# Performance work log

Measured on AMD Instinct MI355X. Metric: run time of the kernel, lower is better.

The kernel has to match this reference:

```python
import jax, jax.numpy as jnp
import numpy as np

N_NODES = 100000
N_EDGES = 1600000
F_IN = 65
HIDDEN = 128
N_CLASSES = 32
NEG_SLOPE = 0.2


def _gat_conv(x0, src, dst, W, a_src, a_dst, b):
    """Single-head GAT-style conv: gather over edges, segment softmax, scatter-add."""
    h = x0 @ W                                  # [N, C]
    s = h @ a_src                                # [N]
    d = h @ a_dst                                # [N]
    e = jax.nn.leaky_relu(s[src] + d[dst], NEG_SLOPE)   # [E]
    m = jax.ops.segment_max(e, dst, num_segments=N_NODES)
    m = jnp.where(jnp.isfinite(m), m, 0.0)
    ex = jnp.exp(e - m[dst])                     # [E]
    denom = jax.ops.segment_sum(ex, dst, num_segments=N_NODES)
    alpha = ex / (denom[dst] + 1e-16)            # [E]
    out = jax.ops.segment_sum(h[src] * alpha[:, None], dst, num_segments=N_NODES)
    return out + b                               # [N, C]


def setup_inputs() -> dict:
    key = jax.random.key(0)
    ks = jax.random.split(key, 12)
    sc_in = 1.0 / np.sqrt(F_IN)
    sc_h = 1.0 / np.sqrt(HIDDEN)
    return {
        "x": jax.random.normal(ks[0], (N_NODES, F_IN), dtype=jnp.float32),
        "edge_index": jax.random.randint(ks[1], (2, N_EDGES), 0, N_NODES, dtype=jnp.int64),
        "W_mlp": jax.random.normal(ks[2], (F_IN, HIDDEN), dtype=jnp.float32) * sc_in,
        "b_mlp": jnp.zeros((HIDDEN,), dtype=jnp.float32),
        "W1": jax.random.normal(ks[3], (HIDDEN, N_CLASSES), dtype=jnp.float32) * sc_h,
        "a1_src": jax.random.normal(ks[4], (N_CLASSES,), dtype=jnp.float32) * 0.1,
        "a1_dst": jax.random.normal(ks[5], (N_CLASSES,), dtype=jnp.float32) * 0.1,
        "b1": jnp.zeros((N_CLASSES,), dtype=jnp.float32),
        "W2": jax.random.normal(ks[6], (HIDDEN, N_CLASSES), dtype=jnp.float32) * sc_h,
        "a2_src": jax.random.normal(ks[7], (N_CLASSES,), dtype=jnp.float32) * 0.1,
        "a2_dst": jax.random.normal(ks[8], (N_CLASSES,), dtype=jnp.float32) * 0.1,
        "b2": jnp.zeros((N_CLASSES,), dtype=jnp.float32),
    }


def reference(x, edge_index, W_mlp, b_mlp, W1, a1_src, a1_dst, b1, W2, a2_src, a2_dst, b2):
    src, dst = edge_index[0], edge_index[1]
    x0 = jax.nn.relu(x @ W_mlp + b_mlp)                      # [N, H]
    x1 = jax.nn.relu(_gat_conv(x0, src, dst, W1, a1_src, a1_dst, b1))  # [N, C]
    # dropout is identity in eval mode
    x2 = _gat_conv(x0, src, dst, W2, a2_src, a2_dst, b2)     # [N, C]
    x3 = jnp.max(x0, axis=-1, keepdims=True)                 # [N, 1]
    lngal_out = jnp.concatenate((x1, x2, x3), axis=-1) + x   # [N, 2C+1] == [N, F]
    return jax.nn.log_softmax(lngal_out, axis=1)
```

## Files before the change

### kernel.cpp

```cpp
#include <hip/hip_runtime.h>
#include <hip/hip_bf16.h>

#define NN 100000
#define NE 1600000
#define FIN 65
#define HID 128
#define NC 32
#define OUTC 65
#define NBUCK 391
#define CHUNKS 400
#define CH 4000
#define ESTRIDE 5120
#define NODE_BLOCKS 1563

typedef __attribute__((ext_vector_type(8))) short s8v;
typedef __attribute__((ext_vector_type(4))) float f4v;
typedef __attribute__((ext_vector_type(2))) float f2v;
#define MFMA16(a, b, c) __builtin_amdgcn_mfma_f32_16x16x32_bf16(a, b, c, 0, 0, 0)

__device__ __forceinline__ float lrelu(float v){ return v > 0.f ? v : 0.2f * v; }
__device__ __forceinline__ short f2bs(float f){
  unsigned u = __float_as_uint(f);
  u += 0x7fffu + ((u >> 16) & 1u);
  return (short)(u >> 16);
}
__device__ __forceinline__ float bfu_lo(unsigned u){ return __uint_as_float(u << 16); }
__device__ __forceinline__ float bfu_hi(unsigned u){ return __uint_as_float(u & 0xffff0000u); }
__device__ __forceinline__ unsigned char f2fp8(float f){
  int p = __builtin_amdgcn_cvt_pk_fp8_f32(f, f, 0, false);
  return (unsigned char)(p & 0xff);
}

__global__ __launch_bounds__(256) void k_prep(
    const float* __restrict__ Wmlp, const float* __restrict__ W1,
    const float* __restrict__ W2, short* __restrict__ wbg,
    int* __restrict__ bcursor)
{
  const int i = blockIdx.x * 256 + threadIdx.x;
  if (blockIdx.x == 0)
    for (int t = threadIdx.x; t < NBUCK; t += 256) bcursor[t] = 0;
  {
    const int j = i & 7, l = (i >> 3) & 63, nt = (i >> 9) & 7, t = i >> 12;
    const int k = t * 32 + ((l >> 4) << 3) + j;
    const int col = (nt << 4) + (l & 15);
    wbg[i] = f2bs(Wmlp[k * HID + col]);
  }
  {
    const int j = i & 7, l = (i >> 3) & 63, nt = (i >> 9) & 3, t = i >> 11;
    const int k = t * 32 + ((l >> 4) << 3) + j;
    const int col = (nt << 4) + (l & 15);
    wbg[8192 + i] = f2bs(col < NC ? W1[k * NC + col] : W2[k * NC + col - NC]);
  }
}

__global__ __launch_bounds__(256) void k_main(
    const float* __restrict__ x, const short* __restrict__ wbg,
    const float* __restrict__ Wmlp, const float* __restrict__ bmlp,
    const float* __restrict__ a1s, const float* __restrict__ a1d,
    const float* __restrict__ a2s, const float* __restrict__ a2d,
    const int* __restrict__ ei,
    unsigned char* __restrict__ hb8,
    float* __restrict__ sd2, float* __restrict__ dd2,
    float* __restrict__ out,
    int* __restrict__ bcursor, int* __restrict__ ebuf)
{
  __shared__ alignas(16) char smem[18944];
  const int tid = threadIdx.x;

  if (blockIdx.x >= NODE_BLOCKS) {
    const int cb = blockIdx.x - NODE_BLOCKS;
    int* lh = (int*)smem;
    int* lbase = lh + NBUCK;
    for (int i = tid; i < NBUCK; i += 256) lh[i] = 0;
    __syncthreads();
    const int4* s4 = (const int4*)ei + cb * (CH / 4);
    const int4* d4 = (const int4*)(ei + NE) + cb * (CH / 4);
    for (int i = tid; i < CH / 4; i += 256) {
      int4 v = d4[i];
      atomicAdd(&lh[v.x >> 8], 1);
      atomicAdd(&lh[v.y >> 8], 1);
      atomicAdd(&lh[v.z >> 8], 1);
      atomicAdd(&lh[v.w >> 8], 1);
    }
    __syncthreads();
    for (int i = tid; i < NBUCK; i += 256) {
      int c = lh[i];
      lbase[i] = c ? (i * ESTRIDE + atomicAdd(&bcursor[i], c)) : 0;
      lh[i] = 0;
    }
    __syncthreads();
    for (int i = tid; i < CH / 4; i += 256) {
      int4 sv = s4[i];
      int4 dv = d4[i];
      int b, r;
      b = dv.x >> 8; r = atomicAdd(&lh[b], 1); ebuf[lbase[b] + r] = (sv.x << 8) | (dv.x & 255);
      b = dv.y >> 8; r = atomicAdd(&lh[b], 1); ebuf[lbase[b] + r] = (sv.y << 8) | (dv.y & 255);
      b = dv.z >> 8; r = atomicAdd(&lh[b], 1); ebuf[lbase[b] + r] = (sv.z << 8) | (dv.z & 255);
      b = dv.w >> 8; r = atomicAdd(&lh[b], 1); ebuf[lbase[b] + r] = (sv.w << 8) | (dv.w & 255);
    }
    return;
  }

  short* x0b = (short*)smem;
  float* w64 = (float*)(smem + 17408);
  float* bmv = (float*)(smem + 17920);
  float* avv = (float*)(smem + 18432);

  const int base = blockIdx.x * 64;
  const int w = tid >> 6, lane = tid & 63;
  const int g = lane >> 4, q = lane & 15;
  const int rowA = w * 16 + q;
  const int rowD0 = w * 16 + g * 4;
  const int nodeA = base + rowA;
  const s8v* wv8 = (const s8v*)wbg;

  float xa[16];
  if (nodeA < NN) {
    const float* xr = x + (size_t)nodeA * FIN + g * 8;
    #pragma unroll
    for (int j = 0; j < 8; ++j) xa[j] = xr[j];
    #pragma unroll
    for (int j = 0; j < 8; ++j) xa[8 + j] = xr[32 + j];
  } else {
    #pragma unroll
    for (int j = 0; j < 16; ++j) xa[j] = 0.f;
  }
  float xc[4];
  #pragma unroll
  for (int r = 0; r < 4; ++r) {
    const int n2 = base + rowD0 + r;
    xc[r] = (n2 < NN) ? x[(size_t)n2 * FIN + 64] : 0.f;
  }

  if (tid < 128) { w64[tid] = Wmlp[64 * HID + tid]; bmv[tid] = bmlp[tid]; }
  else if (tid < 160) {
    const int qq = tid - 128;
    avv[qq] = a1s[qq]; avv[32 + qq] = a1d[qq]; avv[64 + qq] = a2s[qq]; avv[96 + qq] = a2d[qq];
  }
  __syncthreads();

  s8v a0, a1;
  #pragma unroll
  for (int j = 0; j < 8; ++j) { a0[j] = f2bs(xa[j]); a1[j] = f2bs(xa[8 + j]); }

  f4v acc[8];
  #pragma unroll
  for (int nt = 0; nt < 8; ++nt) acc[nt] = (f4v){0.f, 0.f, 0.f, 0.f};
  {
    s8v bb[8];
    #pragma unroll
    for (int nt = 0; nt < 8; ++nt) bb[nt] = wv8[nt * 64 + lane];
    #pragma unroll
    for (int nt = 0; nt < 8; ++nt) acc[nt] = MFMA16(a0, bb[nt], acc[nt]);
    #pragma unroll
    for (int nt = 0; nt < 8; ++nt) bb[nt] = wv8[(8 + nt) * 64 + lane];
    #pragma unroll
    for (int nt = 0; nt < 8; ++nt) acc[nt] = MFMA16(a1, bb[nt], acc[nt]);
  }

  float rmax[4] = {0.f, 0.f, 0.f, 0.f};
  #pragma unroll
  for (int nt = 0; nt < 8; ++nt) {
    const int col = nt * 16 + q;
    const float wvv = w64[col], bv = bmv[col];
    #pragma unroll
    for (int r = 0; r < 4; ++r) {
      const float v = fmaxf(fmaf(xc[r], wvv, acc[nt][r]) + bv, 0.f);
      rmax[r] = fmaxf(rmax[r], v);
      x0b[(rowD0 + r) * 136 + col] = f2bs(v);
    }
  }
  #pragma unroll
  for (int off = 1; off < 16; off <<= 1)
    #pragma unroll
    for (int r = 0; r < 4; ++r) rmax[r] = fmaxf(rmax[r], __shfl_xor(rmax[r], off));
  if (q == 0) {
    #pragma unroll
    for (int r = 0; r < 4; ++r) {
      const int node = base + rowD0 + r;
      if (node < NN) out[(size_t)node * OUTC + 64] = rmax[r];
    }
  }

  s8v af[4];
  #pragma unroll
  for (int t2 = 0; t2 < 4; ++t2)
    af[t2] = *(const s8v*)&x0b[rowA * 136 + t2 * 32 + g * 8];
  f4v hacc[4];
  #pragma unroll
  for (int nt = 0; nt < 4; ++nt) hacc[nt] = (f4v){0.f, 0.f, 0.f, 0.f};
  {
    s8v wt[8];
    #pragma unroll
    for (int i2 = 0; i2 < 8; ++i2) wt[i2] = wv8[1024 + i2 * 64 + lane];
    #pragma unroll
    for (int t2 = 0; t2 < 2; ++t2)
      #pragma unroll
      for (int nt = 0; nt < 4; ++nt)
        hacc[nt] = MFMA16(af[t2], wt[t2 * 4 + nt], hacc[nt]);
    #pragma unroll
    for (int i2 = 0; i2 < 8; ++i2) wt[i2] = wv8[1024 + (8 + i2) * 64 + lane];
    #pragma unroll
    for (int t2 = 0; t2 < 2; ++t2)
      #pragma unroll
      for (int nt = 0; nt < 4; ++nt)
        hacc[nt] = MFMA16(af[2 + t2], wt[t2 * 4 + nt], hacc[nt]);
  }

  float s1p[4], d1p[4], s2p[4], d2p[4];
  #pragma unroll
  for (int r = 0; r < 4; ++r) {
    s1p[r] = hacc[0][r] * avv[q]        + hacc[1][r] * avv[16 + q];
    d1p[r] = hacc[0][r] * avv[32 + q]   + hacc[1][r] * avv[48 + q];
    s2p[r] = hacc[2][r] * avv[64 + q]   + hacc[3][r] * avv[80 + q];
    d2p[r] = hacc[2][r] * avv[96 + q]   + hacc[3][r] * avv[112 + q];
  }
  #pragma unroll
  for (int off = 1; off < 16; off <<= 1) {
    #pragma unroll
    for (int r = 0; r < 4; ++r) {
      s1p[r] += __shfl_xor(s1p[r], off);
      d1p[r] += __shfl_xor(d1p[r], off);
      s2p[r] += __shfl_xor(s2p[r], off);
      d2p[r] += __shfl_xor(d2p[r], off);
    }
  }
  #pragma unroll
  for (int r = 0; r < 4; ++r) {
    const int node = base + rowD0 + r;
    if (node < NN) {
      #pragma unroll
      for (int nt = 0; nt < 4; ++nt)
        hb8[(size_t)node * 64 + nt * 16 + q] = f2fp8(hacc[nt][r]);
      if (q == 0) {
        *(float2*)&sd2[(size_t)node * 2] = make_float2(s1p[r], s2p[r]);
        *(float2*)&dd2[(size_t)node * 2] = make_float2(d1p[r], d2p[r]);
      }
    }
  }
}

__global__ __launch_bounds__(256) void k_csr(const int* __restrict__ bcursor,
                                             const int* __restrict__ ebuf,
                                             int* __restrict__ rpp,
                                             int* __restrict__ csrc)
{
  __shared__ int lh[256];
  __shared__ int wsum[4];
  const int b = blockIdx.x;
  const int e0 = b * ESTRIDE;
  const int cntb = bcursor[b];
  const int t = threadIdx.x;

  lh[t] = 0;
  __syncthreads();
  for (int i = t; i < cntb; i += 256)
    atomicAdd(&lh[ebuf[e0 + i] & 255], 1);
  __syncthreads();

  const int lane = t & 63;
  const int wid = t >> 6;
  int v = lh[t];
  const int orig = v;
  for (int off = 1; off < 64; off <<= 1) {
    int tm = __shfl_up(v, off);
    if (lane >= off) v += tm;
  }
  if (lane == 63) wsum[wid] = v;
  __syncthreads();
  int add = 0;
  for (int ww = 0; ww < wid; ++ww) add += wsum[ww];
  const int ex = v + add - orig;

  const int nb0 = b << 8;
  if (nb0 + t < NN) rpp[nb0 + t] = ((e0 + ex) << 8) | orig;
  __syncthreads();
  lh[t] = ex;
  __syncthreads();
  for (int i = t; i < cntb; i += 256) {
    int p = ebuf[e0 + i];
    int r = atomicAdd(&lh[p & 255], 1);
    csrc[e0 + r] = ((unsigned)p) >> 8;
  }
}

__global__ __launch_bounds__(256) void k_conv(
    const int* __restrict__ rpp, const int* __restrict__ csrc,
    const unsigned char* __restrict__ hb8,
    const float* __restrict__ sd2, const float* __restrict__ dd2,
    const float* __restrict__ x,
    const float* __restrict__ b1, const float* __restrict__ b2,
    float* __restrict__ out)
{
  const int wid = threadIdx.x >> 6;
  const int lane = threadIdx.x & 63;
  const int half = lane >> 5;
  const int hl = lane & 31;
  const int eg = hl >> 4;
  const int cg = hl & 15;
  const int conv = cg >> 3;

  const int node = blockIdx.x * 8 + wid * 2 + half;

  const int rv = rpp[node];
  const int base = ((unsigned)rv) >> 8;
  const int cnt = rv & 255;
  const float2 dnv = *(const float2*)&dd2[(size_t)node * 2];

  const int ch = cg * 4;
  const float* xr = x + (size_t)node * OUTC;
  float* row = out + (size_t)node * OUTC;
  const float4 xr4 = *(const float4*)&xr[ch];
  const float x64v = xr[64];
  const float o64 = row[64];
  const float4 bv = conv ? *(const float4*)&b2[ch - 32] : *(const float4*)&b1[ch];

  float a0 = 0.f, a1 = 0.f, a2 = 0.f, a3 = 0.f;
  float den = 0.f;

  for (int chunk = 0; chunk < cnt; chunk += 32) {
    const int rem = min(cnt - chunk, 32);

    int sE = 0;
    float w1v = 0.f, w2v = 0.f;
    if (hl < rem) {
      sE = csrc[base + chunk + hl];
      const float2 sv = *(const float2*)&sd2[(size_t)sE * 2];
      w1v = __expf(lrelu(sv.x + dnv.x));
      w2v = __expf(lrelu(sv.y + dnv.y));
    }
    float d1 = w1v, d2 = w2v;
    #pragma unroll
    for (int off = 1; off < 32; off <<= 1) {
      d1 += __shfl_xor(d1, off);
      d2 += __shfl_xor(d2, off);
    }
    den += conv ? d2 : d1;

    const int wpk = (int)((((unsigned)(unsigned short)f2bs(w2v)) << 16) |
                           (unsigned)(unsigned short)f2bs(w1v));

    for (int i0 = 0; i0 < rem; i0 += 8) {
      unsigned wps[4];
      unsigned pvs[4];
      #pragma unroll
      for (int u = 0; u < 4; ++u) {
        const int i = i0 + u * 2 + eg;
        const int src = half * 32 + i;
        const int s = __shfl(sE, src);
        wps[u] = (unsigned)__shfl(wpk, src);
        pvs[u] = *(const unsigned*)(hb8 + ((size_t)s << 6) + cg * 4);
      }
      #pragma unroll
      for (int u = 0; u < 4; ++u) {
        const float w = conv ? bfu_hi(wps[u]) : bfu_lo(wps[u]);
        const f2v lo = __builtin_amdgcn_cvt_pk_f32_fp8((int)pvs[u], false);
        const f2v hi = __builtin_amdgcn_cvt_pk_f32_fp8((int)pvs[u], true);
        a0 = fmaf(w, lo[0], a0);
        a1 = fmaf(w, lo[1], a1);
        a2 = fmaf(w, hi[0], a2);
        a3 = fmaf(w, hi[1], a3);
      }
    }
  }

  a0 += __shfl_xor(a0, 16);
  a1 += __shfl_xor(a1, 16);
  a2 += __shfl_xor(a2, 16);
  a3 += __shfl_xor(a3, 16);

  const float rden = 1.f / (den + 1e-16f);
  float v0 = a0 * rden + bv.x;
  float v1 = a1 * rden + bv.y;
  float v2 = a2 * rden + bv.z;
  float v3 = a3 * rden + bv.w;
  if (conv == 0) {
    v0 = fmaxf(v0, 0.f);
    v1 = fmaxf(v1, 0.f);
    v2 = fmaxf(v2, 0.f);
    v3 = fmaxf(v3, 0.f);
  }
  v0 += xr4.x; v1 += xr4.y; v2 += xr4.z; v3 += xr4.w;
  const float v64 = o64 + x64v;

  float mx = fmaxf(fmaxf(v0, v1), fmaxf(v2, v3));
  #pragma unroll
  for (int off = 1; off < 16; off <<= 1) mx = fmaxf(mx, __shfl_xor(mx, off));
  mx = fmaxf(mx, v64);
  float sm = __expf(v0 - mx) + __expf(v1 - mx) + __expf(v2 - mx) + __expf(v3 - mx);
  #pragma unroll
  for (int off = 1; off < 16; off <<= 1) sm += __shfl_xor(sm, off);
  sm += __expf(v64 - mx);
  const float ls = __logf(sm);

  if (eg == 0) {
    *(float4*)&row[ch] = make_float4(v0 - mx - ls, v1 - mx - ls, v2 - mx - ls, v3 - mx - ls);
    if (hl == 0) row[64] = v64 - mx - ls;
  }
}

extern "C" void kernel_launch(void* const* d_in, const int* in_sizes, int n_in,
                              void* d_out, int out_size, void* d_ws, size_t ws_size,
                              hipStream_t stream)
{
  const float* x    = (const float*)d_in[0];
  const int*   ei   = (const int*)d_in[1];
  const float* Wmlp = (const float*)d_in[2];
  const float* bmlp = (const float*)d_in[3];
  const float* W1   = (const float*)d_in[4];
  const float* a1s  = (const float*)d_in[5];
  const float* a1d  = (const float*)d_in[6];
  const float* b1   = (const float*)d_in[7];
  const float* W2   = (const float*)d_in[8];
  const float* a2s  = (const float*)d_in[9];
  const float* a2d  = (const float*)d_in[10];
  const float* b2   = (const float*)d_in[11];
  float* out = (float*)d_out;

  unsigned char* hb8 = (unsigned char*)d_ws;
  float* sd2 = (float*)(hb8 + (size_t)NN * 64);
  float* dd2 = sd2 + (size_t)2 * NN;
  int* ebuf   = (int*)(dd2 + (size_t)2 * NN);
  int* csrc   = ebuf + (size_t)NBUCK * ESTRIDE;
  int* rpp    = csrc + (size_t)NBUCK * ESTRIDE;
  int* bcursor= rpp + NBUCK * 256;
  short* wbg  = (short*)(bcursor + NBUCK);

  k_prep<<<32, 256, 0, stream>>>(Wmlp, W1, W2, wbg, bcursor);

  k_main<<<NODE_BLOCKS + CHUNKS, 256, 0, stream>>>(
      x, wbg, Wmlp, bmlp, a1s, a1d, a2s, a2d, ei,
      hb8, sd2, dd2, out, bcursor, ebuf);

  k_csr<<<NBUCK, 256, 0, stream>>>(bcursor, ebuf, rpp, csrc);

  k_conv<<<NN / 8, 256, 0, stream>>>(rpp, csrc, hb8, sd2, dd2, x, b1, b2, out);
}
```

Measured before the change: 90.94 us.

## Single-pass edge bucketing with LDS staging and schedule edge blocks first

```diff
diff --git a/kernel.cpp b/kernel.cpp
--- a/kernel.cpp
+++ b/kernel.cpp
@@ -12,6 +12,7 @@
 #define CH 4000
 #define ESTRIDE 5120
 #define NODE_BLOCKS 1563
+#define CAP 16
 
 typedef __attribute__((ext_vector_type(8))) short s8v;
 typedef __attribute__((ext_vector_type(4))) float f4v;
@@ -64,39 +65,49 @@
     float* __restrict__ out,
     int* __restrict__ bcursor, int* __restrict__ ebuf)
 {
-  __shared__ alignas(16) char smem[18944];
+  __shared__ alignas(16) char smem[26624];
   const int tid = threadIdx.x;
 
-  if (blockIdx.x >= NODE_BLOCKS) {
-    const int cb = blockIdx.x - NODE_BLOCKS;
+  if (blockIdx.x < CHUNKS) {
+    const int cb = blockIdx.x;
     int* lh = (int*)smem;
-    int* lbase = lh + NBUCK;
+    int* stg = lh + NBUCK;
     for (int i = tid; i < NBUCK; i += 256) lh[i] = 0;
     __syncthreads();
+
     const int4* s4 = (const int4*)ei + cb * (CH / 4);
     const int4* d4 = (const int4*)(ei + NE) + cb * (CH / 4);
     for (int i = tid; i < CH / 4; i += 256) {
-      int4 v = d4[i];
-      atomicAdd(&lh[v.x >> 8], 1);
-      atomicAdd(&lh[v.y >> 8], 1);
-      atomicAdd(&lh[v.z >> 8], 1);
-      atomicAdd(&lh[v.w >> 8], 1);
+      const int4 sv = s4[i];
+      const int4 dv = d4[i];
+      int b, r, p;
+      b = dv.x >> 8; p = (sv.x << 8) | (dv.x & 255);
+      r = atomicAdd(&lh[b], 1);
+      if (r < CAP) stg[b * CAP + r] = p;
+      else ebuf[b * ESTRIDE + atomicAdd(&bcursor[b], 1)] = p;
+      b = dv.y >> 8; p = (sv.y << 8) | (dv.y & 255);
+      r = atomicAdd(&lh[b], 1);
+      if (r < CAP) stg[b * CAP + r] = p;
+      else ebuf[b * ESTRIDE + atomicAdd(&bcursor[b], 1)] = p;
+      b = dv.z >> 8; p = (sv.z << 8) | (dv.z & 255);
+      r = atomicAdd(&lh[b], 1);
+      if (r < CAP) stg[b * CAP + r] = p;
+      else ebuf[b * ESTRIDE + atomicAdd(&bcursor[b], 1)] = p;
+      b = dv.w >> 8; p = (sv.w << 8) | (dv.w & 255);
+      r = atomicAdd(&lh[b], 1);
+      if (r < CAP) stg[b * CAP + r] = p;
+      else ebuf[b * ESTRIDE + atomicAdd(&bcursor[b], 1)] = p;
     }
     __syncthreads();
+
+    const int rot = (cb * 89) % NBUCK;
     for (int i = tid; i < NBUCK; i += 256) {
-      int c = lh[i];
-      lbase[i] = c ? (i * ESTRIDE + atomicAdd(&bcursor[i], c)) : 0;
-      lh[i] = 0;
-    }
-    __syncthreads();
-    for (int i = tid; i < CH / 4; i += 256) {
-      int4 sv = s4[i];
-      int4 dv = d4[i];
-      int b, r;
-      b = dv.x >> 8; r = atomicAdd(&lh[b], 1); ebuf[lbase[b] + r] = (sv.x << 8) | (dv.x & 255);
-      b = dv.y >> 8; r = atomicAdd(&lh[b], 1); ebuf[lbase[b] + r] = (sv.y << 8) | (dv.y & 255);
-      b = dv.z >> 8; r = atomicAdd(&lh[b], 1); ebuf[lbase[b] + r] = (sv.z << 8) | (dv.z & 255);
-      b = dv.w >> 8; r = atomicAdd(&lh[b], 1); ebuf[lbase[b] + r] = (sv.w << 8) | (dv.w & 255);
+      int bb = i + rot; if (bb >= NBUCK) bb -= NBUCK;
+      const int c = min(lh[bb], CAP);
+      if (c) {
+        int gbase = bb * ESTRIDE + atomicAdd(&bcursor[bb], c);
+        for (int j = 0; j < c; ++j) ebuf[gbase + j] = stg[bb * CAP + j];
+      }
     }
     return;
   }
@@ -106,7 +117,7 @@
   float* bmv = (float*)(smem + 17920);
   float* avv = (float*)(smem + 18432);
 
-  const int base = blockIdx.x * 64;
+  const int base = (blockIdx.x - CHUNKS) * 64;
   const int w = tid >> 6, lane = tid & 63;
   const int g = lane >> 4, q = lane & 15;
   const int rowA = w * 16 + q;
@@ -131,6 +142,9 @@
     const int n2 = base + rowD0 + r;
     xc[r] = (n2 < NN) ? x[(size_t)n2 * FIN + 64] : 0.f;
   }
+  s8v bb[8];
+  #pragma unroll
+  for (int nt = 0; nt < 8; ++nt) bb[nt] = wv8[nt * 64 + lane];
 
   if (tid < 128) { w64[tid] = Wmlp[64 * HID + tid]; bmv[tid] = bmlp[tid]; }
   else if (tid < 160) {
@@ -147,9 +161,6 @@
   #pragma unroll
   for (int nt = 0; nt < 8; ++nt) acc[nt] = (f4v){0.f, 0.f, 0.f, 0.f};
   {
-    s8v bb[8];
-    #pragma unroll
-    for (int nt = 0; nt < 8; ++nt) bb[nt] = wv8[nt * 64 + lane];
     #pragma unroll
     for (int nt = 0; nt < 8; ++nt) acc[nt] = MFMA16(a0, bb[nt], acc[nt]);
     #pragma unroll
```

Result: slower. 107.4 us (+18.0%).

## Replace global bucket atomics with per-chunk local sort and count/offset tables

Applied to the files above, without the earlier changes.

```diff
diff --git a/kernel.cpp b/kernel.cpp
--- a/kernel.cpp
+++ b/kernel.cpp
@@ -30,15 +30,24 @@
   int p = __builtin_amdgcn_cvt_pk_fp8_f32(f, f, 0, false);
   return (unsigned char)(p & 0xff);
 }
+__device__ __forceinline__ void scan512incl(int* a){
+  const int t = threadIdx.x;
+  #pragma unroll
+  for (int s = 1; s < 512; s <<= 1) {
+    const int v0 = (t >= s) ? a[t - s] : 0;
+    const int v1 = (t + 256 - s >= 0) ? a[t + 256 - s] : 0;
+    __syncthreads();
+    a[t] += v0;
+    a[t + 256] += v1;
+    __syncthreads();
+  }
+}
 
 __global__ __launch_bounds__(256) void k_prep(
     const float* __restrict__ Wmlp, const float* __restrict__ W1,
-    const float* __restrict__ W2, short* __restrict__ wbg,
-    int* __restrict__ bcursor)
+    const float* __restrict__ W2, short* __restrict__ wbg)
 {
   const int i = blockIdx.x * 256 + threadIdx.x;
-  if (blockIdx.x == 0)
-    for (int t = threadIdx.x; t < NBUCK; t += 256) bcursor[t] = 0;
   {
     const int j = i & 7, l = (i >> 3) & 63, nt = (i >> 9) & 7, t = i >> 12;
     const int k = t * 32 + ((l >> 4) << 3) + j;
@@ -62,42 +71,51 @@
     unsigned char* __restrict__ hb8,
     float* __restrict__ sd2, float* __restrict__ dd2,
     float* __restrict__ out,
-    int* __restrict__ bcursor, int* __restrict__ ebuf)
+    int* __restrict__ ebuf, int* __restrict__ cntT, int* __restrict__ offT)
 {
-  __shared__ alignas(16) char smem[18944];
+  __shared__ alignas(16) char smem[20480];
   const int tid = threadIdx.x;
 
   if (blockIdx.x >= NODE_BLOCKS) {
     const int cb = blockIdx.x - NODE_BLOCKS;
-    int* lh = (int*)smem;
-    int* lbase = lh + NBUCK;
-    for (int i = tid; i < NBUCK; i += 256) lh[i] = 0;
-    __syncthreads();
+    int* srt = (int*)smem;
+    int* lh  = srt + 4096;
+    int* sc  = lh + 512;
+    for (int i = tid; i < 512; i += 256) lh[i] = 0;
+    __syncthreads();
+
     const int4* s4 = (const int4*)ei + cb * (CH / 4);
     const int4* d4 = (const int4*)(ei + NE) + cb * (CH / 4);
     for (int i = tid; i < CH / 4; i += 256) {
-      int4 v = d4[i];
+      const int4 v = d4[i];
       atomicAdd(&lh[v.x >> 8], 1);
       atomicAdd(&lh[v.y >> 8], 1);
       atomicAdd(&lh[v.z >> 8], 1);
       atomicAdd(&lh[v.w >> 8], 1);
     }
     __syncthreads();
+    for (int i = tid; i < 512; i += 256) sc[i] = lh[i];
+    __syncthreads();
+    scan512incl(sc);
     for (int i = tid; i < NBUCK; i += 256) {
-      int c = lh[i];
-      lbase[i] = c ? (i * ESTRIDE + atomicAdd(&bcursor[i], c)) : 0;
-      lh[i] = 0;
+      const int c = lh[i];
+      const int ex = sc[i] - c;
+      cntT[cb * NBUCK + i] = c;
+      offT[cb * NBUCK + i] = ex;
+      sc[i] = ex;
     }
     __syncthreads();
     for (int i = tid; i < CH / 4; i += 256) {
-      int4 sv = s4[i];
-      int4 dv = d4[i];
+      const int4 sv = s4[i];
+      const int4 dv = d4[i];
       int b, r;
-      b = dv.x >> 8; r = atomicAdd(&lh[b], 1); ebuf[lbase[b] + r] = (sv.x << 8) | (dv.x & 255);
-      b = dv.y >> 8; r = atomicAdd(&lh[b], 1); ebuf[lbase[b] + r] = (sv.y << 8) | (dv.y & 255);
-      b = dv.z >> 8; r = atomicAdd(&lh[b], 1); ebuf[lbase[b] + r] = (sv.z << 8) | (dv.z & 255);
-      b = dv.w >> 8; r = atomicAdd(&lh[b], 1); ebuf[lbase[b] + r] = (sv.w << 8) | (dv.w & 255);
-    }
+      b = dv.x >> 8; r = atomicAdd(&sc[b], 1); srt[r] = (sv.x << 8) | (dv.x & 255);
+      b = dv.y >> 8; r = atomicAdd(&sc[b], 1); srt[r] = (sv.y << 8) | (dv.y & 255);
+      b = dv.z >> 8; r = atomicAdd(&sc[b], 1); srt[r] = (sv.z << 8) | (dv.z & 255);
+      b = dv.w >> 8; r = atomicAdd(&sc[b], 1); srt[r] = (sv.w << 8) | (dv.w & 255);
+    }
+    __syncthreads();
+    for (int i = tid; i < CH; i += 256) ebuf[cb * CH + i] = srt[i];
     return;
   }
 
@@ -131,6 +149,9 @@
     const int n2 = base + rowD0 + r;
     xc[r] = (n2 < NN) ? x[(size_t)n2 * FIN + 64] : 0.f;
   }
+  s8v bb[8];
+  #pragma unroll
+  for (int nt = 0; nt < 8; ++nt) bb[nt] = wv8[nt * 64 + lane];
 
   if (tid < 128) { w64[tid] = Wmlp[64 * HID + tid]; bmv[tid] = bmlp[tid]; }
   else if (tid < 160) {
@@ -147,9 +168,6 @@
   #pragma unroll
   for (int nt = 0; nt < 8; ++nt) acc[nt] = (f4v){0.f, 0.f, 0.f, 0.f};
   {
-    s8v bb[8];
-    #pragma unroll
-    for (int nt = 0; nt < 8; ++nt) bb[nt] = wv8[nt * 64 + lane];
     #pragma unroll
     for (int nt = 0; nt < 8; ++nt) acc[nt] = MFMA16(a0, bb[nt], acc[nt]);
     #pragma unroll
@@ -240,22 +258,42 @@
   }
 }
 
-__global__ __launch_bounds__(256) void k_csr(const int* __restrict__ bcursor,
-                                             const int* __restrict__ ebuf,
-                                             int* __restrict__ rpp,
-                                             int* __restrict__ csrc)
+__global__ __launch_bounds__(256) void k_csr(
+    const int* __restrict__ cntT, const int* __restrict__ offT,
+    const int* __restrict__ ebuf,
+    int* __restrict__ rpp, int* __restrict__ csrc)
 {
+  __shared__ int eL[4608];
+  __shared__ int ccnt[512];
+  __shared__ int cpos[512];
+  __shared__ int coff[CHUNKS];
   __shared__ int lh[256];
   __shared__ int wsum[4];
   const int b = blockIdx.x;
-  const int e0 = b * ESTRIDE;
-  const int cntb = bcursor[b];
   const int t = threadIdx.x;
 
+  for (int i = t; i < 512; i += 256) {
+    const int c = (i < CHUNKS) ? cntT[i * NBUCK + b] : 0;
+    ccnt[i] = c;
+    cpos[i] = c;
+  }
+  for (int i = t; i < CHUNKS; i += 256) coff[i] = offT[i * NBUCK + b];
+  __syncthreads();
+  scan512incl(cpos);
+  const int cntb = cpos[CHUNKS - 1];
+
+  for (int c = t; c < CHUNKS; c += 256) {
+    const int n = ccnt[c];
+    const int dst0 = cpos[c] - n;
+    const int src0 = c * CH + coff[c];
+    for (int j = 0; j < n; ++j) eL[dst0 + j] = ebuf[src0 + j];
+  }
+  __syncthreads();
+
   lh[t] = 0;
   __syncthreads();
   for (int i = t; i < cntb; i += 256)
-    atomicAdd(&lh[ebuf[e0 + i] & 255], 1);
+    atomicAdd(&lh[eL[i] & 255], 1);
   __syncthreads();
 
   const int lane = t & 63;
@@ -273,13 +311,14 @@
   const int ex = v + add - orig;
 
   const int nb0 = b << 8;
+  const int e0 = b * ESTRIDE;
   if (nb0 + t < NN) rpp[nb0 + t] = ((e0 + ex) << 8) | orig;
   __syncthreads();
   lh[t] = ex;
   __syncthreads();
   for (int i = t; i < cntb; i += 256) {
-    int p = ebuf[e0 + i];
-    int r = atomicAdd(&lh[p & 255], 1);
+    const int p = eL[i];
+    const int r = atomicAdd(&lh[p & 255], 1);
     csrc[e0 + r] = ((unsigned)p) >> 8;
   }
 }
@@ -421,18 +460,19 @@
   float* sd2 = (float*)(hb8 + (size_t)NN * 64);
   float* dd2 = sd2 + (size_t)2 * NN;
   int* ebuf   = (int*)(dd2 + (size_t)2 * NN);
-  int* csrc   = ebuf + (size_t)NBUCK * ESTRIDE;
+  int* csrc   = ebuf + NE;
   int* rpp    = csrc + (size_t)NBUCK * ESTRIDE;
-  int* bcursor= rpp + NBUCK * 256;
-  short* wbg  = (short*)(bcursor + NBUCK);
-
-  k_prep<<<32, 256, 0, stream>>>(Wmlp, W1, W2, wbg, bcursor);
+  int* cntT   = rpp + NBUCK * 256;
+  int* offT   = cntT + CHUNKS * NBUCK;
+  short* wbg  = (short*)(offT + CHUNKS * NBUCK);
+
+  k_prep<<<32, 256, 0, stream>>>(Wmlp, W1, W2, wbg);
 
   k_main<<<NODE_BLOCKS + CHUNKS, 256, 0, stream>>>(
       x, wbg, Wmlp, bmlp, a1s, a1d, a2s, a2d, ei,
-      hb8, sd2, dd2, out, bcursor, ebuf);
-
-  k_csr<<<NBUCK, 256, 0, stream>>>(bcursor, ebuf, rpp, csrc);
+      hb8, sd2, dd2, out, ebuf, cntT, offT);
+
+  k_csr<<<NBUCK, 256, 0, stream>>>(cntT, offT, ebuf, rpp, csrc);
 
   k_conv<<<NN / 8, 256, 0, stream>>>(rpp, csrc, hb8, sd2, dd2, x, b1, b2, out);
 }
```

Measured after the change: 88.26 us (median of 2 runs). -2.9%, faster.
